# Kernel optimization log

Measured on AMD Instinct MI355X. Metric: run time of the kernel, lower is better.

The kernel has to match this reference:

```python
import jax, jax.numpy as jnp
import numpy as np

N = 40000      # nodes
D = 64         # nnodefeatures
DEG = 32       # avg in-degree
E = N * DEG    # edges
G = 200        # graphs in batch
ATT = 64       # attention_size
HID = 128      # cls_hidden_dim
NCLS = 6
NLAYERS = 3


def setup_inputs() -> dict:
    key = jax.random.key(0)
    ks = jax.random.split(key, 8)
    s = 0.05
    x = jax.random.normal(ks[0], (N, D), dtype=jnp.float32)
    row = jax.random.randint(ks[1], (E,), 0, N, dtype=jnp.int32)
    # every node appears as a target exactly DEG times -> no zero degrees
    col = jnp.repeat(jnp.arange(N, dtype=jnp.int32), DEG)
    edge_index = jnp.stack([row, col])
    batch = jnp.repeat(jnp.arange(G, dtype=jnp.int32), N // G)
    W_lin = jax.random.normal(ks[2], (D, D), jnp.float32) * s
    b_lin = jnp.zeros((D,), jnp.float32)
    W_att = jax.random.normal(ks[3], (ATT, 2 * D), jnp.float32) * s
    a_vec = jnp.ones((ATT, 1), jnp.float32)  # torch.ones init
    W1 = jax.random.normal(ks[4], (HID, D), jnp.float32) * s
    b1 = jnp.zeros((HID,), jnp.float32)
    W2 = jax.random.normal(ks[5], (NCLS, HID), jnp.float32) * s
    b2 = jnp.zeros((NCLS,), jnp.float32)
    return dict(x=x, W_lin=W_lin, b_lin=b_lin, W_att=W_att, a_vec=a_vec,
                W1=W1, b1=b1, W2=W2, b2=b2,
                edge_index=edge_index, batch=batch, n_graphs=G)


def _gnn_layer(x, row, col, W_lin, b_lin, W_att, a_vec):
    n = x.shape[0]
    deg = jnp.sqrt(jax.ops.segment_sum(jnp.ones_like(col, dtype=x.dtype), col, num_segments=n))
    deg = jnp.where(jnp.isinf(deg), jnp.zeros_like(deg), deg)  # deg[deg==inf]=0
    norm = deg[row] * deg[col]                                  # [E]
    x_j = x[row]                                                # [E, D] gather source
    x_i = x[col]                                                # [E, D] gather target
    att_in = jnp.concatenate([x_j, x_i], axis=-1)               # [E, 2D]
    score = jnp.exp((att_in @ W_att.T) @ a_vec)                 # [E, 1]
    att_norm = jax.ops.segment_sum(score, col, num_segments=n)  # [N, 1] (scatter by edge_index[1])
    att = score / att_norm[row]                                 # gathered at edge_index[0] (faithful)
    m = ((x_j * att) @ W_lin.T + b_lin) / norm[:, None]         # [E, D]
    out = jax.ops.segment_sum(m, col, num_segments=n)           # aggregate by target
    return jax.nn.selu(out)


def reference(x, W_lin, b_lin, W_att, a_vec, W1, b1, W2, b2, edge_index, batch, n_graphs):
    row, col = edge_index[0], edge_index[1]
    # Faithful to original: the loop re-applies the layer to the ORIGINAL x each time
    for _ in range(NLAYERS):
        h = _gnn_layer(x, row, col, W_lin, b_lin, W_att, a_vec)
    sums = jax.ops.segment_sum(h, batch, num_segments=n_graphs)
    counts = jax.ops.segment_sum(jnp.ones((x.shape[0],), x.dtype), batch, num_segments=n_graphs)
    pooled = sums / counts[:, None]                              # global_mean_pool
    hcls = jax.nn.selu(pooled @ W1.T + b1)
    logits = hcls @ W2.T + b2
    return jax.nn.softmax(logits, axis=-1)
```

## Files before the change

kernel.cpp:

```cpp
#include <hip/hip_runtime.h>
#include <hip/hip_bf16.h>
#include <stdint.h>

#define N_NODES 40000
#define D_FEAT 64
#define DEG 32
#define E_EDGES (N_NODES * DEG)
#define G_GRAPHS 200
#define NPG 200
#define ATT_SZ 64
#define HID 128
#define NCLS 6
#define XS 69

__device__ __forceinline__ float selu_f(float x) {
    const float scale = 1.0507009873554805f;
    const float alpha = 1.6732632423543772f;
    return scale * (x > 0.f ? x : alpha * (__expf(x) - 1.f));
}

__device__ __forceinline__ uint32_t f2bf(float f) {
    uint32_t u = __builtin_bit_cast(uint32_t, f);
    return (u + 0x7fffu + ((u >> 16) & 1u)) >> 16;
}
__device__ __forceinline__ float bflo(uint32_t u) { return __builtin_bit_cast(float, u << 16); }
__device__ __forceinline__ float bfhi(uint32_t u) { return __builtin_bit_cast(float, u & 0xffff0000u); }

__global__ __launch_bounds__(128) void k_w(const float* __restrict__ Watt,
                                           const float* __restrict__ avec,
                                           float* __restrict__ wbuf) {
    int t = threadIdx.x;
    float s = 0.f;
#pragma unroll
    for (int k = 0; k < ATT_SZ; ++k) s += avec[k] * Watt[k * 128 + t];
    wbuf[t] = s;
}

__global__ __launch_bounds__(256) void k_node(const float* __restrict__ x,
                                              const float* __restrict__ Wlin,
                                              const float* __restrict__ wbuf,
                                              float* __restrict__ P,
                                              float* __restrict__ Q,
                                              uint32_t* __restrict__ yb,
                                              float* __restrict__ pool) {
    __shared__ float xs[160 * XS];
    __shared__ float ws[64 * XS];
    __shared__ float ws_w[128];
    int tid = threadIdx.x;
    int n0 = blockIdx.x * 160;
    if (blockIdx.x < 50) pool[blockIdx.x * 256 + tid] = 0.f;

    const float4* x4 = (const float4*)(x + (size_t)n0 * 64);
    const float4* W4 = (const float4*)Wlin;
#pragma unroll
    for (int s = 0; s < 10; ++s) {
        int idx = tid + s * 256, r = idx >> 4, kk = idx & 15;
        *(float4*)&xs[r * XS + kk * 4] = x4[idx];
    }
#pragma unroll
    for (int s = 0; s < 4; ++s) {
        int idx = tid + s * 256, r = idx >> 4, kk = idx & 15;
        *(float4*)&ws[r * XS + kk * 4] = W4[idx];
    }
    if (tid < 128) ws_w[tid] = wbuf[tid];
    __syncthreads();

    if (tid < 160) {
        float s1 = 0.f, s2 = 0.f;
#pragma unroll 8
        for (int k = 0; k < 64; ++k) {
            float xv = xs[tid * XS + k];
            s1 += xv * ws_w[k];
            s2 += xv * ws_w[64 + k];
        }
        P[n0 + tid] = __expf(s1);
        Q[n0 + tid] = __expf(s2);
    }

    int tm = tid >> 4, tf = tid & 15;
    float acc[10][4];
#pragma unroll
    for (int i = 0; i < 10; ++i)
#pragma unroll
        for (int j = 0; j < 4; ++j) acc[i][j] = 0.f;
#pragma unroll 2
    for (int kk = 0; kk < 16; ++kk) {
        float4 wv[4];
#pragma unroll
        for (int j = 0; j < 4; ++j) wv[j] = *(const float4*)&ws[(4 * tf + j) * XS + kk * 4];
#pragma unroll
        for (int i = 0; i < 10; ++i) {
            float4 xv = *(const float4*)&xs[(tm + 16 * i) * XS + kk * 4];
#pragma unroll
            for (int j = 0; j < 4; ++j)
                acc[i][j] += xv.x * wv[j].x + xv.y * wv[j].y
                           + xv.z * wv[j].z + xv.w * wv[j].w;
        }
    }
#pragma unroll
    for (int i = 0; i < 10; ++i) {
        int m = n0 + tm + 16 * i;
        uint32_t p0 = f2bf(acc[i][0]) | (f2bf(acc[i][1]) << 16);
        uint32_t p1 = f2bf(acc[i][2]) | (f2bf(acc[i][3]) << 16);
        *(uint2*)&yb[(size_t)m * 32 + tf * 2] = make_uint2(p0, p1);
    }
}

__global__ __launch_bounds__(256) void k_edges(const int* __restrict__ row,
                                               const float* __restrict__ P,
                                               const float* __restrict__ Q,
                                               float* __restrict__ V) {
    int e = blockIdx.x * 256 + threadIdx.x;
    float p = P[row[e]];
#pragma unroll
    for (int off = 16; off; off >>= 1)
        p += __shfl_xor(p, off, 32);
    if ((threadIdx.x & 31) == 0) {
        int n = e >> 5;
        V[n] = P[n] / (Q[n] * p);
    }
}

__global__ __launch_bounds__(256) void k_agg(const int* __restrict__ row,
                                             const float* __restrict__ V,
                                             const float* __restrict__ Q,
                                             const uint32_t* __restrict__ yb,
                                             const float* __restrict__ blin,
                                             float* __restrict__ pool) {
    __shared__ float2 meta[1024];
    int tid = threadIdx.x;
    int n0 = blockIdx.x * 32;

    int4 r4 = ((const int4*)(row + (size_t)n0 * 32))[tid];
    meta[4 * tid + 0] = make_float2(V[r4.x], __builtin_bit_cast(float, r4.x << 7));
    meta[4 * tid + 1] = make_float2(V[r4.y], __builtin_bit_cast(float, r4.y << 7));
    meta[4 * tid + 2] = make_float2(V[r4.z], __builtin_bit_cast(float, r4.z << 7));
    meta[4 * tid + 3] = make_float2(V[r4.w], __builtin_bit_cast(float, r4.w << 7));
    __syncthreads();

    int wv = tid >> 6, lane = tid & 63;
    int q = lane >> 4, fi = lane & 15;
    float4 bl4 = ((const float4*)blin)[fi];
    int nw0 = n0 + wv * 8;
    float4 pacc = make_float4(0.f, 0.f, 0.f, 0.f);
    const char* ybc = (const char*)yb;
#pragma unroll 1
    for (int nn = 0; nn < 8; ++nn) {
        int n = nw0 + nn;
        int base = (wv * 8 + nn) * 32;
        float4 a = make_float4(0.f, 0.f, 0.f, 0.f);
#pragma unroll
        for (int s = 0; s < 8; ++s) {
            float2 m = meta[base + s * 4 + q];
            uint32_t rbyte = __builtin_bit_cast(uint32_t, m.y);
            uint2 u = *(const uint2*)(ybc + rbyte + fi * 8);
            a.x += m.x * bflo(u.x);
            a.y += m.x * bfhi(u.x);
            a.z += m.x * bflo(u.y);
            a.w += m.x * bfhi(u.y);
        }
        a.x += __shfl_xor(a.x, 16, 64); a.x += __shfl_xor(a.x, 32, 64);
        a.y += __shfl_xor(a.y, 16, 64); a.y += __shfl_xor(a.y, 32, 64);
        a.z += __shfl_xor(a.z, 16, 64); a.z += __shfl_xor(a.z, 32, 64);
        a.w += __shfl_xor(a.w, 16, 64); a.w += __shfl_xor(a.w, 32, 64);
        float qn = Q[n] * (1.f / 32.f);
        pacc.x += selu_f(qn * a.x + bl4.x);
        pacc.y += selu_f(qn * a.y + bl4.y);
        pacc.z += selu_f(qn * a.z + bl4.z);
        pacc.w += selu_f(qn * a.w + bl4.w);
    }
    if (q == 0) {
        int g = nw0 / NPG;
        float* pp = &pool[g * 64 + 4 * fi];
        atomicAdd(pp + 0, pacc.x);
        atomicAdd(pp + 1, pacc.y);
        atomicAdd(pp + 2, pacc.z);
        atomicAdd(pp + 3, pacc.w);
    }
}

__global__ __launch_bounds__(128) void k_cls(const float* __restrict__ pool,
                                             const float* __restrict__ W1,
                                             const float* __restrict__ b1,
                                             const float* __restrict__ W2,
                                             const float* __restrict__ b2,
                                             float* __restrict__ out) {
    __shared__ float ps[64];
    __shared__ float hc[HID];
    __shared__ float lg[NCLS];
    int t = threadIdx.x, g = blockIdx.x;
    if (t < 64) ps[t] = pool[g * 64 + t] * (1.f / NPG);
    __syncthreads();
    float s = b1[t];
    const float4* w14 = (const float4*)(W1 + t * 64);
    const float4* ps4 = (const float4*)ps;
#pragma unroll
    for (int kk = 0; kk < 16; ++kk) {
        float4 w = w14[kk], p = ps4[kk];
        s += w.x * p.x; s += w.y * p.y; s += w.z * p.z; s += w.w * p.w;
    }
    hc[t] = selu_f(s);
    __syncthreads();
    if (t < NCLS) {
        float l = b2[t];
        const float4* w24 = (const float4*)(W2 + t * 128);
        const float4* hc4 = (const float4*)hc;
        for (int kk = 0; kk < 32; ++kk) {
            float4 w = w24[kk], h = hc4[kk];
            l += w.x * h.x; l += w.y * h.y; l += w.z * h.z; l += w.w * h.w;
        }
        lg[t] = l;
    }
    __syncthreads();
    if (t == 0) {
        float m = lg[0];
        for (int c = 1; c < NCLS; ++c) m = fmaxf(m, lg[c]);
        float ex[NCLS], sum = 0.f;
        for (int c = 0; c < NCLS; ++c) { ex[c] = __expf(lg[c] - m); sum += ex[c]; }
        for (int c = 0; c < NCLS; ++c) out[g * NCLS + c] = ex[c] / sum;
    }
}

extern "C" void kernel_launch(void* const* d_in, const int* in_sizes, int n_in,
                              void* d_out, int out_size, void* d_ws, size_t ws_size,
                              hipStream_t stream) {
    const float* x    = (const float*)d_in[0];
    const float* Wlin = (const float*)d_in[1];
    const float* blin = (const float*)d_in[2];
    const float* Watt = (const float*)d_in[3];
    const float* avec = (const float*)d_in[4];
    const float* W1   = (const float*)d_in[5];
    const float* b1   = (const float*)d_in[6];
    const float* W2   = (const float*)d_in[7];
    const float* b2   = (const float*)d_in[8];
    const int*   row  = (const int*)d_in[9];
    float* out = (float*)d_out;

    float* P    = (float*)d_ws;
    float* Q    = P + N_NODES;
    float* V    = Q + N_NODES;
    float* pool = V + N_NODES;
    float* wbuf = pool + G_GRAPHS * 64;
    uint32_t* yb = (uint32_t*)(wbuf + 128);

    k_w<<<1, 128, 0, stream>>>(Watt, avec, wbuf);
    k_node<<<N_NODES / 160, 256, 0, stream>>>(x, Wlin, wbuf, P, Q, yb, pool);
    k_edges<<<E_EDGES / 256, 256, 0, stream>>>(row, P, Q, V);
    k_agg<<<N_NODES / 32, 256, 0, stream>>>(row, V, Q, yb, blin, pool);
    k_cls<<<G_GRAPHS, 128, 0, stream>>>(pool, W1, b1, W2, b2, out);
}
```

Before: 131.7 us.

## Aggregate raw fp16 features first, apply linear transform after aggregation

Reorders the layer so that neighbour features (stored as fp16 instead of bf16 projected features) are aggregated with attention weights first, and the W_lin matmul plus bias and SELU is applied per node afterwards in a new kernel. The node prep kernel becomes a lightweight conversion plus attention-score pass, while a new k_mm kernel does the matmul on aggregated rows and pools. This adds an extra fp32 N×64 round trip through global memory and one more kernel launch, in exchange for a simpler prep kernel and better fp16 precision.

```diff
diff --git a/kernel.cpp b/kernel.cpp
--- a/kernel.cpp
+++ b/kernel.cpp
@@ -1,5 +1,5 @@
 #include <hip/hip_runtime.h>
-#include <hip/hip_bf16.h>
+#include <hip/hip_fp16.h>
 #include <stdint.h>
 
 #define N_NODES 40000
@@ -11,7 +11,6 @@
 #define ATT_SZ 64
 #define HID 128
 #define NCLS 6
-#define XS 69
 
 __device__ __forceinline__ float selu_f(float x) {
     const float scale = 1.0507009873554805f;
@@ -19,12 +18,6 @@
     return scale * (x > 0.f ? x : alpha * (__expf(x) - 1.f));
 }
 
-__device__ __forceinline__ uint32_t f2bf(float f) {
-    uint32_t u = __builtin_bit_cast(uint32_t, f);
-    return (u + 0x7fffu + ((u >> 16) & 1u)) >> 16;
-}
-__device__ __forceinline__ float bflo(uint32_t u) { return __builtin_bit_cast(float, u << 16); }
-__device__ __forceinline__ float bfhi(uint32_t u) { return __builtin_bit_cast(float, u & 0xffff0000u); }
 
 __global__ __launch_bounds__(128) void k_w(const float* __restrict__ Watt,
                                            const float* __restrict__ avec,
@@ -36,74 +29,44 @@
     wbuf[t] = s;
 }
 
-__global__ __launch_bounds__(256) void k_node(const float* __restrict__ x,
-                                              const float* __restrict__ Wlin,
+__global__ __launch_bounds__(256) void k_prep(const float* __restrict__ x,
                                               const float* __restrict__ wbuf,
                                               float* __restrict__ P,
                                               float* __restrict__ Q,
-                                              uint32_t* __restrict__ yb,
+                                              uint32_t* __restrict__ xb,
                                               float* __restrict__ pool) {
-    __shared__ float xs[160 * XS];
-    __shared__ float ws[64 * XS];
-    __shared__ float ws_w[128];
+    __shared__ float w_s[128];
     int tid = threadIdx.x;
-    int n0 = blockIdx.x * 160;
     if (blockIdx.x < 50) pool[blockIdx.x * 256 + tid] = 0.f;
-
-    const float4* x4 = (const float4*)(x + (size_t)n0 * 64);
-    const float4* W4 = (const float4*)Wlin;
-#pragma unroll
-    for (int s = 0; s < 10; ++s) {
-        int idx = tid + s * 256, r = idx >> 4, kk = idx & 15;
-        *(float4*)&xs[r * XS + kk * 4] = x4[idx];
-    }
-#pragma unroll
-    for (int s = 0; s < 4; ++s) {
-        int idx = tid + s * 256, r = idx >> 4, kk = idx & 15;
-        *(float4*)&ws[r * XS + kk * 4] = W4[idx];
-    }
-    if (tid < 128) ws_w[tid] = wbuf[tid];
-    __syncthreads();
-
-    if (tid < 160) {
-        float s1 = 0.f, s2 = 0.f;
-#pragma unroll 8
-        for (int k = 0; k < 64; ++k) {
-            float xv = xs[tid * XS + k];
-            s1 += xv * ws_w[k];
-            s2 += xv * ws_w[64 + k];
-        }
-        P[n0 + tid] = __expf(s1);
-        Q[n0 + tid] = __expf(s2);
-    }
-
-    int tm = tid >> 4, tf = tid & 15;
-    float acc[10][4];
-#pragma unroll
-    for (int i = 0; i < 10; ++i)
-#pragma unroll
-        for (int j = 0; j < 4; ++j) acc[i][j] = 0.f;
-#pragma unroll 2
-    for (int kk = 0; kk < 16; ++kk) {
-        float4 wv[4];
-#pragma unroll
-        for (int j = 0; j < 4; ++j) wv[j] = *(const float4*)&ws[(4 * tf + j) * XS + kk * 4];
-#pragma unroll
-        for (int i = 0; i < 10; ++i) {
-            float4 xv = *(const float4*)&xs[(tm + 16 * i) * XS + kk * 4];
-#pragma unroll
-            for (int j = 0; j < 4; ++j)
-                acc[i][j] += xv.x * wv[j].x + xv.y * wv[j].y
-                           + xv.z * wv[j].z + xv.w * wv[j].w;
-        }
-    }
-#pragma unroll
-    for (int i = 0; i < 10; ++i) {
-        int m = n0 + tm + 16 * i;
-        uint32_t p0 = f2bf(acc[i][0]) | (f2bf(acc[i][1]) << 16);
-        uint32_t p1 = f2bf(acc[i][2]) | (f2bf(acc[i][3]) << 16);
-        *(uint2*)&yb[(size_t)m * 32 + tf * 2] = make_uint2(p0, p1);
-    }
+    if (tid < 128) w_s[tid] = wbuf[tid];
+    __syncthreads();
+
+    int wv = tid >> 6, lane = tid & 63;
+    int nl = lane >> 3, part = lane & 7;
+    int n = blockIdx.x * 32 + wv * 8 + nl;
+    const float4* xr = (const float4*)(x + (size_t)n * 64);
+    float4 f0 = xr[part * 2], f1 = xr[part * 2 + 1];
+
+    int k0 = part * 8;
+    float s1 = f0.x * w_s[k0];
+    s1 += f0.y * w_s[k0 + 1]; s1 += f0.z * w_s[k0 + 2]; s1 += f0.w * w_s[k0 + 3];
+    s1 += f1.x * w_s[k0 + 4]; s1 += f1.y * w_s[k0 + 5];
+    s1 += f1.z * w_s[k0 + 6]; s1 += f1.w * w_s[k0 + 7];
+    float s2 = f0.x * w_s[64 + k0];
+    s2 += f0.y * w_s[64 + k0 + 1]; s2 += f0.z * w_s[64 + k0 + 2]; s2 += f0.w * w_s[64 + k0 + 3];
+    s2 += f1.x * w_s[64 + k0 + 4]; s2 += f1.y * w_s[64 + k0 + 5];
+    s2 += f1.z * w_s[64 + k0 + 6]; s2 += f1.w * w_s[64 + k0 + 7];
+    s1 += __shfl_xor(s1, 1, 64); s1 += __shfl_xor(s1, 2, 64); s1 += __shfl_xor(s1, 4, 64);
+    s2 += __shfl_xor(s2, 1, 64); s2 += __shfl_xor(s2, 2, 64); s2 += __shfl_xor(s2, 4, 64);
+    if (part == 0) { P[n] = __expf(s1); Q[n] = __expf(s2); }
+
+    __half2 h0 = __float22half2_rn(make_float2(f0.x, f0.y));
+    __half2 h1 = __float22half2_rn(make_float2(f0.z, f0.w));
+    __half2 h2 = __float22half2_rn(make_float2(f1.x, f1.y));
+    __half2 h3 = __float22half2_rn(make_float2(f1.z, f1.w));
+    ((uint4*)xb)[(size_t)n * 8 + part] =
+        make_uint4(__builtin_bit_cast(uint32_t, h0), __builtin_bit_cast(uint32_t, h1),
+                   __builtin_bit_cast(uint32_t, h2), __builtin_bit_cast(uint32_t, h3));
 }
 
 __global__ __launch_bounds__(256) void k_edges(const int* __restrict__ row,
@@ -123,10 +86,8 @@
 
 __global__ __launch_bounds__(256) void k_agg(const int* __restrict__ row,
                                              const float* __restrict__ V,
-                                             const float* __restrict__ Q,
-                                             const uint32_t* __restrict__ yb,
-                                             const float* __restrict__ blin,
-                                             float* __restrict__ pool) {
+                                             const uint32_t* __restrict__ xb,
+                                             float* __restrict__ agg) {
     __shared__ float2 meta[1024];
     int tid = threadIdx.x;
     int n0 = blockIdx.x * 32;
@@ -140,10 +101,8 @@
 
     int wv = tid >> 6, lane = tid & 63;
     int q = lane >> 4, fi = lane & 15;
-    float4 bl4 = ((const float4*)blin)[fi];
     int nw0 = n0 + wv * 8;
-    float4 pacc = make_float4(0.f, 0.f, 0.f, 0.f);
-    const char* ybc = (const char*)yb;
+    const char* xbc = (const char*)xb;
 #pragma unroll 1
     for (int nn = 0; nn < 8; ++nn) {
         int n = nw0 + nn;
@@ -153,29 +112,69 @@
         for (int s = 0; s < 8; ++s) {
             float2 m = meta[base + s * 4 + q];
             uint32_t rbyte = __builtin_bit_cast(uint32_t, m.y);
-            uint2 u = *(const uint2*)(ybc + rbyte + fi * 8);
-            a.x += m.x * bflo(u.x);
-            a.y += m.x * bfhi(u.x);
-            a.z += m.x * bflo(u.y);
-            a.w += m.x * bfhi(u.y);
+            uint2 u = *(const uint2*)(xbc + rbyte + fi * 8);
+            float2 g0 = __half22float2(__builtin_bit_cast(__half2, u.x));
+            float2 g1 = __half22float2(__builtin_bit_cast(__half2, u.y));
+            a.x += m.x * g0.x;
+            a.y += m.x * g0.y;
+            a.z += m.x * g1.x;
+            a.w += m.x * g1.y;
         }
         a.x += __shfl_xor(a.x, 16, 64); a.x += __shfl_xor(a.x, 32, 64);
         a.y += __shfl_xor(a.y, 16, 64); a.y += __shfl_xor(a.y, 32, 64);
         a.z += __shfl_xor(a.z, 16, 64); a.z += __shfl_xor(a.z, 32, 64);
         a.w += __shfl_xor(a.w, 16, 64); a.w += __shfl_xor(a.w, 32, 64);
-        float qn = Q[n] * (1.f / 32.f);
-        pacc.x += selu_f(qn * a.x + bl4.x);
-        pacc.y += selu_f(qn * a.y + bl4.y);
-        pacc.z += selu_f(qn * a.z + bl4.z);
-        pacc.w += selu_f(qn * a.w + bl4.w);
-    }
-    if (q == 0) {
-        int g = nw0 / NPG;
-        float* pp = &pool[g * 64 + 4 * fi];
-        atomicAdd(pp + 0, pacc.x);
-        atomicAdd(pp + 1, pacc.y);
-        atomicAdd(pp + 2, pacc.z);
-        atomicAdd(pp + 3, pacc.w);
+        if (q == 0) *(float4*)&agg[(size_t)n * 64 + 4 * fi] = a;
+    }
+}
+
+__global__ __launch_bounds__(256) void k_mm(const float* __restrict__ agg,
+                                            const float* __restrict__ Wlin,
+                                            const float* __restrict__ Q,
+                                            const float* __restrict__ blin,
+                                            float* __restrict__ pool) {
+    __shared__ float W_s[64 * 65];
+    int tid = threadIdx.x;
+#pragma unroll
+    for (int s = 0; s < 16; ++s) {
+        int idx = tid + s * 256;
+        W_s[(idx >> 6) * 65 + (idx & 63)] = Wlin[idx];
+    }
+    __syncthreads();
+
+    int wv = tid >> 6, lane = tid & 63;
+    int nl = lane >> 3, dg = lane & 7;
+    int n = blockIdx.x * 32 + wv * 8 + nl;
+    const float4* ar = (const float4*)(agg + (size_t)n * 64);
+    float4 av[16];
+#pragma unroll
+    for (int i = 0; i < 16; ++i) av[i] = ar[i];
+    float qn = Q[n] * (1.f / 32.f);
+
+    float hv[8];
+#pragma unroll
+    for (int j = 0; j < 8; ++j) {
+        const float* wr = &W_s[(dg * 8 + j) * 65];
+        float s = 0.f;
+#pragma unroll
+        for (int i = 0; i < 16; ++i) {
+            float4 a4 = av[i];
+            s += a4.x * wr[4 * i];     s += a4.y * wr[4 * i + 1];
+            s += a4.z * wr[4 * i + 2]; s += a4.w * wr[4 * i + 3];
+        }
+        hv[j] = selu_f(qn * s + blin[dg * 8 + j]);
+    }
+#pragma unroll
+    for (int j = 0; j < 8; ++j) {
+        hv[j] += __shfl_xor(hv[j], 8, 64);
+        hv[j] += __shfl_xor(hv[j], 16, 64);
+        hv[j] += __shfl_xor(hv[j], 32, 64);
+    }
+    if (nl == 0) {
+        int g = (blockIdx.x * 32 + wv * 8) / NPG;
+        float* pp = &pool[g * 64 + dg * 8];
+#pragma unroll
+        for (int j = 0; j < 8; ++j) atomicAdd(pp + j, hv[j]);
     }
 }
 
@@ -241,11 +240,13 @@
     float* V    = Q + N_NODES;
     float* pool = V + N_NODES;
     float* wbuf = pool + G_GRAPHS * 64;
-    uint32_t* yb = (uint32_t*)(wbuf + 128);
+    uint32_t* xb = (uint32_t*)(wbuf + 128);
+    float* agg  = (float*)(xb + (size_t)N_NODES * 32);
 
     k_w<<<1, 128, 0, stream>>>(Watt, avec, wbuf);
-    k_node<<<N_NODES / 160, 256, 0, stream>>>(x, Wlin, wbuf, P, Q, yb, pool);
+    k_prep<<<N_NODES / 32, 256, 0, stream>>>(x, wbuf, P, Q, xb, pool);
     k_edges<<<E_EDGES / 256, 256, 0, stream>>>(row, P, Q, V);
-    k_agg<<<N_NODES / 32, 256, 0, stream>>>(row, V, Q, yb, blin, pool);
+    k_agg<<<N_NODES / 32, 256, 0, stream>>>(row, V, xb, agg);
+    k_mm<<<N_NODES / 32, 256, 0, stream>>>(agg, Wlin, Q, blin, pool);
     k_cls<<<G_GRAPHS, 128, 0, stream>>>(pool, W1, b1, W2, b2, out);
 }
```

New measurement: 155.6 us. 18.2% more time.
